# Kernel optimization log

Hardware: AMD Instinct MI355X
Metric: run time of the kernel (lower is better)

The kernel has to match this reference:

```python
import jax, jax.numpy as jnp
import numpy as np

DIM = 192          # token dim
INNER = 288        # round4(1.5*DIM)
NH_Q = 72          # headwise-proj heads (INNER // qkv_block_size)
DH_Q = 4           # per-head dim of q/k/v projections
NH_M = 4           # mLSTM heads (= qkv_block_size)
DH_M = 72          # INNER // NH_M
H, W = 32, 32
S = H * W
B = 8
KS = 3             # conv kernel size
EPS = 1e-6
LN_EPS = 1e-5


def setup_inputs() -> dict:
    key = jax.random.key(0)
    ks = jax.random.split(key, 12)
    sc = 0.02
    return {
        "x": jax.random.normal(ks[0], (B, S, DIM), jnp.float32),
        "proj_up_w": jax.random.normal(ks[1], (2 * INNER, DIM), jnp.float32) * sc,
        "q_w": jax.random.normal(ks[2], (NH_Q, DH_Q, DH_Q), jnp.float32) * sc,
        "k_w": jax.random.normal(ks[3], (NH_Q, DH_Q, DH_Q), jnp.float32) * sc,
        "v_w": jax.random.normal(ks[4], (NH_Q, DH_Q, DH_Q), jnp.float32) * sc,
        "conv_w": jax.random.normal(ks[5], (KS, KS, 1, INNER), jnp.float32) * sc,  # depthwise HWIO
        "ig_w": jax.random.normal(ks[6], (NH_M, 3 * INNER), jnp.float32) * sc,
        "ig_b": jax.random.normal(ks[7], (NH_M,), jnp.float32) * 0.1,
        "fg_w": jax.random.normal(ks[8], (NH_M, 3 * INNER), jnp.float32) * sc,
        "fg_b": jnp.linspace(3.0, 6.0, NH_M, dtype=jnp.float32),  # original fgate bias init
        "norm_w": jnp.ones((INNER,), jnp.float32),
        "skip": jnp.ones((INNER,), jnp.float32),
        "proj_down_w": jax.random.normal(ks[9], (DIM, INNER), jnp.float32) * sc,
    }


def _headwise(x, w):
    # x: (B,S,INNER), w: (NH_Q, DH_Q, DH_Q); block-diagonal linear per head
    xh = x.reshape(*x.shape[:-1], NH_Q, DH_Q)
    return jnp.einsum("bshd,hod->bsho", xh, w).reshape(x.shape)


def _mlstm_parallel(q, k, v, ig, fg):
    # q,k,v: (B,NH,S,DH); ig,fg: (B,NH,S) gate preactivations
    Ss, DH = q.shape[2], q.shape[3]
    logf = jax.nn.log_sigmoid(fg)                 # (B,NH,S)
    lfc = jnp.cumsum(logf, axis=-1)               # (B,NH,S)
    logF = lfc[..., :, None] - lfc[..., None, :]  # (B,NH,S,S): sum of logf over (j, i]
    mask = jnp.tril(jnp.ones((Ss, Ss), bool))
    logD = jnp.where(mask, logF + ig[..., None, :], -jnp.inf)
    maxD = jnp.max(logD, axis=-1, keepdims=True)  # (B,NH,S,1)
    Dm = jnp.exp(logD - maxD)
    qk = jnp.einsum("bnsd,bntd->bnst", q, k) / jnp.sqrt(jnp.float32(DH))
    Cm = qk * Dm
    normalizer = jnp.maximum(jnp.abs(Cm.sum(-1, keepdims=True)), jnp.exp(-maxD))
    return jnp.einsum("bnst,bntd->bnsd", Cm / (normalizer + EPS), v)


def reference(x, proj_up_w, q_w, k_w, v_w, conv_w, ig_w, ig_b, fg_w, fg_b,
              norm_w, skip, proj_down_w):
    Bb, Ss, _ = x.shape
    y = x @ proj_up_w.T                               # (B,S,2*INNER)
    x_m, z = y[..., :INNER], y[..., INNER:]
    # depthwise 2d conv over the (H,W) token grid
    xc = x_m.reshape(Bb, H, W, INNER)
    xc = jax.lax.conv_general_dilated(
        xc, conv_w, (1, 1), "SAME",
        dimension_numbers=("NHWC", "HWIO", "NHWC"), feature_group_count=INNER)
    xc = xc.reshape(Bb, Ss, INNER)
    xa = jax.nn.silu(xc)
    q = _headwise(xa, q_w)
    k = _headwise(xa, k_w)
    v = _headwise(x_m, v_w)
    gate_in = jnp.concatenate([q, k, v], axis=-1)      # (B,S,3*INNER)
    ig = (gate_in @ ig_w.T + ig_b).transpose(0, 2, 1)  # (B,NH_M,S)
    fg = (gate_in @ fg_w.T + fg_b).transpose(0, 2, 1)
    qh = q.reshape(Bb, Ss, NH_M, DH_M).transpose(0, 2, 1, 3)
    kh = k.reshape(Bb, Ss, NH_M, DH_M).transpose(0, 2, 1, 3)
    vh = v.reshape(Bb, Ss, NH_M, DH_M).transpose(0, 2, 1, 3)
    h = _mlstm_parallel(qh, kh, vh, ig, fg)            # (B,NH_M,S,DH_M)
    # per-head layernorm (group norm with NH_M groups), weight per channel
    mu = h.mean(-1, keepdims=True)
    var = h.var(-1, keepdims=True)
    hn = (h - mu) / jnp.sqrt(var + LN_EPS)
    hn = hn * norm_w.reshape(NH_M, 1, DH_M)[None]
    hn = hn.transpose(0, 2, 1, 3).reshape(Bb, Ss, INNER)
    h_skip = hn + skip * xa
    h_state = h_skip * jax.nn.silu(z)
    return h_state @ proj_down_w.T
```

## Files before the change

### kernel.cpp

```cpp
#include <hip/hip_runtime.h>
#include <math.h>

#define B_ 8
#define S_ 1024
#define INNER_ 288
#define NHM_ 4
#define DHM_ 72
#define H_ 32
#define W_ 32

typedef unsigned short ushort_t;
typedef unsigned int uint_t;
typedef __bf16 bf16x8 __attribute__((ext_vector_type(8)));
typedef float f32x4 __attribute__((ext_vector_type(4)));

__device__ __forceinline__ ushort_t f2bf(float f) {
  union { float f; unsigned u; } v; v.f = f;
  unsigned r = v.u + 0x7FFF + ((v.u >> 16) & 1);
  return (ushort_t)(r >> 16);
}
__device__ __forceinline__ float bf2f(ushort_t u) {
  union { unsigned u; float f; } v; v.u = ((unsigned)u) << 16;
  return v.f;
}
__device__ __forceinline__ void gl16(const void* g, void* l) {
  __builtin_amdgcn_global_load_lds(
      (const __attribute__((address_space(1))) void*)g,
      (__attribute__((address_space(3))) void*)l, 16, 0, 0);
}

__global__ __launch_bounds__(256) void cvt_swz_kernel(
    const float* __restrict__ src, ushort_t* __restrict__ dst, int K, int KPAD) {
  const int idx = blockIdx.x * 256 + threadIdx.x;
  const int k = idx % KPAD, m = idx / KPAD;
  const float v = (k < K) ? src[(size_t)m * K + k] : 0.f;
  dst[(size_t)m * KPAD + (k & ~63) + ((k & 63) ^ ((m & 7) << 3))] = f2bf(v);
}

template<int KT>
__global__ __launch_bounds__(256) void gemm_bf16(
    const ushort_t* __restrict__ A, const ushort_t* __restrict__ Bw,
    float* __restrict__ C, int N) {
  __shared__ __align__(16) ushort_t As[2][128 * 64];
  __shared__ __align__(16) ushort_t Bs[2][64 * 64];
  const int tid = threadIdx.x, lane = tid & 63, wv = tid >> 6;
  const int wm = wv >> 1, wn = wv & 1;
  const int cl = lane & 15, rowb = lane >> 4;
  const int m0 = blockIdx.y * 128, n0 = blockIdx.x * 64;
  const char* Ab = (const char*)A;
  const char* Bb = (const char*)Bw;

  auto stage = [&](int buf, int kt) {
    for (int u = wv; u < 24; u += 4) {
      if (u < 16) {
        const int o = u * 1024 + lane * 16;
        const int r = o >> 7, c = o & 127;
        gl16(Ab + ((size_t)(m0 + r) * KT + kt) * 128 + c, (char*)As[buf] + u * 1024);
      } else {
        const int o = (u - 16) * 1024 + lane * 16;
        const int r = o >> 7, c = o & 127;
        gl16(Bb + ((size_t)(n0 + r) * KT + kt) * 128 + c, (char*)Bs[buf] + (u - 16) * 1024);
      }
    }
  };

  f32x4 acc[4][2];
#pragma unroll
  for (int mi = 0; mi < 4; ++mi)
#pragma unroll
    for (int nj = 0; nj < 2; ++nj) acc[mi][nj] = (f32x4){0.f, 0.f, 0.f, 0.f};

  stage(0, 0);
  __syncthreads();
  for (int kt = 0; kt < KT; ++kt) {
    const int cur = kt & 1;
    if (kt + 1 < KT) stage(cur ^ 1, kt + 1);
#pragma unroll
    for (int ks = 0; ks < 2; ++ks) {
      bf16x8 af[4], bfr[2];
#pragma unroll
      for (int mi = 0; mi < 4; ++mi) {
        const int row = wm * 64 + mi * 16 + cl;
        af[mi] = *(const bf16x8*)((const char*)As[cur] + row * 128 +
                                  ((2 * (ks * 32 + rowb * 8)) ^ ((row & 7) << 4)));
      }
#pragma unroll
      for (int nj = 0; nj < 2; ++nj) {
        const int row = wn * 32 + nj * 16 + cl;
        bfr[nj] = *(const bf16x8*)((const char*)Bs[cur] + row * 128 +
                                   ((2 * (ks * 32 + rowb * 8)) ^ ((row & 7) << 4)));
      }
#pragma unroll
      for (int mi = 0; mi < 4; ++mi)
#pragma unroll
        for (int nj = 0; nj < 2; ++nj)
          acc[mi][nj] = __builtin_amdgcn_mfma_f32_16x16x32_bf16(af[mi], bfr[nj], acc[mi][nj], 0, 0, 0);
    }
    __syncthreads();
  }
#pragma unroll
  for (int mi = 0; mi < 4; ++mi)
#pragma unroll
    for (int i = 0; i < 4; ++i) {
      const size_t m = m0 + wm * 64 + mi * 16 + rowb * 4 + i;
#pragma unroll
      for (int nj = 0; nj < 2; ++nj)
        C[m * N + n0 + wn * 32 + nj * 16 + cl] = acc[mi][nj][i];
    }
}

__global__ __launch_bounds__(256) void conv_silu_kernel(
    const float* __restrict__ y, const float* __restrict__ cw, float* __restrict__ xa) {
  const int idx = blockIdx.x * 256 + threadIdx.x;
  const int c4 = idx % 72;
  const int p = idx / 72;
  const int c = c4 * 4;
  const int xx = p & 31, yy = (p >> 5) & 31, b = p >> 10;
  float4 acc = {0.f, 0.f, 0.f, 0.f};
#pragma unroll
  for (int ky = 0; ky < 3; ++ky) {
    const int iy = yy + ky - 1;
    if (iy < 0 || iy >= H_) continue;
#pragma unroll
    for (int kx = 0; kx < 3; ++kx) {
      const int ix = xx + kx - 1;
      if (ix < 0 || ix >= W_) continue;
      const float4 v = *(const float4*)&y[((size_t)((b << 10) + (iy << 5) + ix)) * 576 + c];
      const float4 w = *(const float4*)&cw[(ky * 3 + kx) * INNER_ + c];
      acc.x += v.x * w.x; acc.y += v.y * w.y; acc.z += v.z * w.z; acc.w += v.w * w.w;
    }
  }
  float4 o;
  o.x = acc.x / (1.f + __expf(-acc.x));
  o.y = acc.y / (1.f + __expf(-acc.y));
  o.z = acc.z / (1.f + __expf(-acc.z));
  o.w = acc.w / (1.f + __expf(-acc.w));
  *(float4*)&xa[(size_t)p * INNER_ + c] = o;
}

__global__ __launch_bounds__(256) void headwise_kernel(
    const float* __restrict__ y, const float* __restrict__ xa,
    const float* __restrict__ qw, const float* __restrict__ kw, const float* __restrict__ vw,
    ushort_t* __restrict__ qg, ushort_t* __restrict__ kg, ushort_t* __restrict__ vg) {
  const int idx = blockIdx.x * 256 + threadIdx.x;
  const int g = idx & 31, r = idx >> 5;
  const int s = r & 1023, bn = r >> 10, b = bn >> 2, n = bn & 3;
  const int swz = (r & 7) << 3;
  ushort_t* qrow = qg + (size_t)r * 128;
  ushort_t* krow = kg + (size_t)r * 128;
  if (g >= 18) {
    const int d0 = 72 + (g - 18) * 4;
    const ushort4 z = {0, 0, 0, 0};
    *(ushort4*)&qrow[d0 ^ swz] = z;
    *(ushort4*)&krow[d0 ^ swz] = z;
    return;
  }
  const int hq = n * 18 + g;
  const int p = (b << 10) + s;
  const float4 xav = *(const float4*)&xa[(size_t)p * INNER_ + hq * 4];
  const float4 xmv = *(const float4*)&y[(size_t)p * 576 + hq * 4];
  float q[4], k2[4], v[4];
#pragma unroll
  for (int o = 0; o < 4; ++o) {
    const float4 wq = *(const float4*)&qw[hq * 16 + o * 4];
    const float4 wk = *(const float4*)&kw[hq * 16 + o * 4];
    const float4 wv4 = *(const float4*)&vw[hq * 16 + o * 4];
    q[o]  = wq.x * xav.x + wq.y * xav.y + wq.z * xav.z + wq.w * xav.w;
    k2[o] = wk.x * xav.x + wk.y * xav.y + wk.z * xav.z + wk.w * xav.w;
    v[o]  = wv4.x * xmv.x + wv4.y * xmv.y + wv4.z * xmv.z + wv4.w * xmv.w;
  }
  ushort4 uq = {f2bf(q[0]), f2bf(q[1]), f2bf(q[2]), f2bf(q[3])};
  ushort4 uk = {f2bf(k2[0]), f2bf(k2[1]), f2bf(k2[2]), f2bf(k2[3])};
  ushort4 uv = {f2bf(v[0]), f2bf(v[1]), f2bf(v[2]), f2bf(v[3])};
  *(ushort4*)&qrow[(g * 4) ^ swz] = uq;
  *(ushort4*)&krow[(g * 4) ^ swz] = uk;
  *(ushort4*)&vg[(size_t)r * 72 + g * 4] = uv;
}

__global__ __launch_bounds__(256) void vtrans_kernel(
    const ushort_t* __restrict__ vg, ushort_t* __restrict__ vtg) {
  __shared__ ushort_t T[64][82];
  const int bn = blockIdx.x >> 4, tt = blockIdx.x & 15;
  const int s0 = tt << 6, tid = threadIdx.x;
  const uint_t* v32 = (const uint_t*)vg;
  for (int i = tid; i < 64 * 36; i += 256) {
    const int rr = i / 36, c2 = i % 36;
    *(uint_t*)&T[rr][c2 * 2] = v32[((size_t)(bn * 1024 + s0 + rr)) * 36 + c2];
  }
  __syncthreads();
  char* outb = (char*)(vtg + ((size_t)(bn * 16 + tt)) * 5120);
  for (int i = tid; i < 80 * 32; i += 256) {
    const int d = i >> 5, m = i & 31;
    uint_t val;
    if (d < 72) val = (uint_t)T[2 * m][d] | ((uint_t)T[2 * m + 1][d] << 16);
    else val = (d == 72) ? 0x3F803F80u : 0u;
    *(uint_t*)(outb + d * 128 + ((m * 4) ^ ((d & 7) << 4))) = val;
  }
}

__global__ __launch_bounds__(256) void gates_kernel(
    const ushort_t* __restrict__ qg, const ushort_t* __restrict__ kg, const ushort_t* __restrict__ vg,
    const float* __restrict__ igw, const float* __restrict__ igb,
    const float* __restrict__ fgw, const float* __restrict__ fgb,
    float* __restrict__ ig, float* __restrict__ fg) {
  const int gw = (blockIdx.x * 256 + threadIdx.x) >> 6;
  const int lane = threadIdx.x & 63;
  const int b = gw >> 10, s = gw & 1023;
  float iacc[4] = {}, facc[4] = {};
  for (int j = lane; j < 864; j += 64) {
    const int part = j / INNER_;
    const int c = j - part * INNER_;
    const int n = c / DHM_, d = c % DHM_;
    const size_t row = (size_t)(b * 4 + n) * 1024 + s;
    ushort_t u;
    if (part == 2)      u = vg[row * 72 + d];
    else {
      const size_t si = row * 128 + (d ^ ((row & 7) << 3));
      u = (part == 0) ? qg[si] : kg[si];
    }
    const float gv = bf2f(u);
#pragma unroll
    for (int nn = 0; nn < 4; ++nn) {
      iacc[nn] += gv * igw[nn * 864 + j];
      facc[nn] += gv * fgw[nn * 864 + j];
    }
  }
#pragma unroll
  for (int off = 32; off >= 1; off >>= 1) {
#pragma unroll
    for (int nn = 0; nn < 4; ++nn) {
      iacc[nn] += __shfl_xor(iacc[nn], off);
      facc[nn] += __shfl_xor(facc[nn], off);
    }
  }
  if (lane == 0) {
#pragma unroll
    for (int nn = 0; nn < 4; ++nn) {
      ig[((size_t)b * NHM_ + nn) * S_ + s] = iacc[nn] + igb[nn];
      fg[((size_t)b * NHM_ + nn) * S_ + s] = facc[nn] + fgb[nn];
    }
  }
}

__global__ __launch_bounds__(256) void scan_kernel(
    const float* __restrict__ fg, const float* __restrict__ ig,
    float* __restrict__ lfc, float* __restrict__ g, float* __restrict__ Mb) {
  __shared__ float sd[256];
  const int bn = blockIdx.x;
  const int tid = threadIdx.x;
  const float* fgp = &fg[(size_t)bn * S_];
  const float* igp = &ig[(size_t)bn * S_];
  float lf[4];
#pragma unroll
  for (int i = 0; i < 4; ++i) {
    const float f = fgp[tid * 4 + i];
    lf[i] = (f >= 0.f) ? -log1pf(expf(-f)) : (f - log1pf(expf(f)));
  }
  float p[4];
  p[0] = lf[0]; p[1] = p[0] + lf[1]; p[2] = p[1] + lf[2]; p[3] = p[2] + lf[3];
  sd[tid] = p[3];
  __syncthreads();
  for (int off = 1; off < 256; off <<= 1) {
    const float v = (tid >= off) ? sd[tid - off] : 0.f;
    __syncthreads();
    sd[tid] += v;
    __syncthreads();
  }
  const float excl = sd[tid] - p[3];
  float l[4];
#pragma unroll
  for (int i = 0; i < 4; ++i) {
    l[i] = excl + p[i];
    lfc[(size_t)bn * S_ + tid * 4 + i] = l[i];
  }
  float gv[4], pm[4];
#pragma unroll
  for (int i = 0; i < 4; ++i) gv[i] = igp[tid * 4 + i] - l[i];
  pm[0] = gv[0];
#pragma unroll
  for (int i = 1; i < 4; ++i) pm[i] = fmaxf(pm[i - 1], gv[i]);
  __syncthreads();
  sd[tid] = pm[3];
  __syncthreads();
  for (int off = 1; off < 256; off <<= 1) {
    const float v = (tid >= off) ? sd[tid - off] : -INFINITY;
    __syncthreads();
    sd[tid] = fmaxf(sd[tid], v);
    __syncthreads();
  }
  const float exclm = (tid > 0) ? sd[tid - 1] : -INFINITY;
#pragma unroll
  for (int i = 0; i < 4; ++i) {
    g[(size_t)bn * S_ + tid * 4 + i] = gv[i];
    Mb[(size_t)bn * S_ + tid * 4 + i] = fmaxf(exclm, pm[i]);
  }
}

__global__ __launch_bounds__(256) void mlstm_mfma(
    const ushort_t* __restrict__ qg, const ushort_t* __restrict__ kg,
    const ushort_t* __restrict__ vtg,
    const float* __restrict__ gb, const float* __restrict__ Mb, const float* __restrict__ lfc,
    float* __restrict__ hb) {
  __shared__ __align__(16) ushort_t Ks[2][64 * 128];
  __shared__ __align__(16) ushort_t Vt[2][80 * 64];
  __shared__ __align__(16) ushort_t Ps[64 * 72];
  __shared__ float gs[1024];
  __shared__ float Ms_s[64], en_s[64];
  const int bi = blockIdx.x;
  const int bn = bi & 31;
  const int j = (bi >> 5) & 7;
  const int st = (bi >> 8) ? (15 - j) : j;
  const int s0 = st << 6;
  const int tid = threadIdx.x, lane = tid & 63, wv = tid >> 6;
  const int cl = lane & 15, rowb = lane >> 4;
  const char* kb = (const char*)(kg + (size_t)bn * 1024 * 128);
  const char* vtb = (const char*)(vtg + (size_t)bn * 16 * 5120);

  auto stage = [&](int buf, int tt) {
    const char* ks = kb + (size_t)tt * (64 * 256);
    const char* vs = vtb + (size_t)tt * 10240;
    for (int u = wv; u < 26; u += 4) {
      if (u < 16) gl16(ks + u * 1024 + lane * 16, (char*)Ks[buf] + u * 1024);
      else        gl16(vs + (u - 16) * 1024 + lane * 16, (char*)Vt[buf] + (u - 16) * 1024);
    }
  };

  stage(0, 0);
  *(float4*)&gs[tid * 4] = *(const float4*)&gb[(size_t)bn * S_ + tid * 4];
  if (tid < 64) {
    const float m = Mb[(size_t)bn * S_ + s0 + tid];
    Ms_s[tid] = m;
    en_s[tid] = __expf(-(lfc[(size_t)bn * S_ + s0 + tid] + m));
  }
  const int qrow = bn * 1024 + s0 + 16 * wv + cl;
  const ushort_t* qp = qg + (size_t)qrow * 128;
  const int qx = (qrow & 7) << 3;
  bf16x8 qf[3];
#pragma unroll
  for (int kk = 0; kk < 3; ++kk) qf[kk] = *(const bf16x8*)&qp[(kk * 32 + rowb * 8) ^ qx];

  f32x4 accv[5];
#pragma unroll
  for (int n0 = 0; n0 < 5; ++n0) accv[n0] = (f32x4){0.f, 0.f, 0.f, 0.f};
  const float rsc = 0.11785113019775793f;
  const int srl0 = 16 * wv + 4 * rowb;
  __syncthreads();

  for (int tt = 0; tt < st; ++tt) {
    const int cur = tt & 1;
    stage(cur ^ 1, tt + 1);
    const int t0 = tt << 6;
    f32x4 qk[4];
#pragma unroll
    for (int n0 = 0; n0 < 4; ++n0) qk[n0] = (f32x4){0.f, 0.f, 0.f, 0.f};
#pragma unroll
    for (int kk = 0; kk < 3; ++kk) {
#pragma unroll
      for (int n0 = 0; n0 < 4; ++n0) {
        const int rl = n0 * 16 + cl;
        const bf16x8 b = *(const bf16x8*)((const char*)Ks[cur] + rl * 256 +
                                          ((2 * (kk * 32 + rowb * 8)) ^ ((rl & 7) << 4)));
        qk[n0] = __builtin_amdgcn_mfma_f32_16x16x32_bf16(qf[kk], b, qk[n0], 0, 0, 0);
      }
    }
#pragma unroll
    for (int n0 = 0; n0 < 4; ++n0) {
      const float gtv = gs[t0 + n0 * 16 + cl];
#pragma unroll
      for (int i = 0; i < 4; ++i) {
        const float w = qk[n0][i] * rsc * __expf(gtv - Ms_s[srl0 + i]);
        Ps[(srl0 + i) * 72 + n0 * 16 + cl] = f2bf(w);
      }
    }
#pragma unroll
    for (int k0 = 0; k0 < 64; k0 += 32) {
      const bf16x8 a = *(const bf16x8*)&Ps[(16 * wv + cl) * 72 + k0 + rowb * 8];
#pragma unroll
      for (int n0 = 0; n0 < 5; ++n0) {
        const int d = n0 * 16 + cl;
        const bf16x8 b = *(const bf16x8*)((const char*)Vt[cur] + d * 128 +
                                          ((2 * (k0 + rowb * 8)) ^ ((d & 7) << 4)));
        accv[n0] = __builtin_amdgcn_mfma_f32_16x16x32_bf16(a, b, accv[n0], 0, 0, 0);
      }
    }
    __syncthreads();
  }
  {
    const int cur = st & 1;
    f32x4 qk[4];
#pragma unroll
    for (int n0 = 0; n0 < 4; ++n0) qk[n0] = (f32x4){0.f, 0.f, 0.f, 0.f};
#pragma unroll
    for (int kk = 0; kk < 3; ++kk) {
#pragma unroll
      for (int n0 = 0; n0 < 4; ++n0) {
        const int rl = n0 * 16 + cl;
        const bf16x8 b = *(const bf16x8*)((const char*)Ks[cur] + rl * 256 +
                                          ((2 * (kk * 32 + rowb * 8)) ^ ((rl & 7) << 4)));
        qk[n0] = __builtin_amdgcn_mfma_f32_16x16x32_bf16(qf[kk], b, qk[n0], 0, 0, 0);
      }
    }
#pragma unroll
    for (int n0 = 0; n0 < 4; ++n0) {
      const int tc = n0 * 16 + cl;
      const float gtv = gs[s0 + tc];
#pragma unroll
      for (int i = 0; i < 4; ++i) {
        const int srl = srl0 + i;
        const float w = (tc <= srl) ? qk[n0][i] * rsc * __expf(gtv - Ms_s[srl]) : 0.f;
        Ps[srl * 72 + n0 * 16 + cl] = f2bf(w);
      }
    }
#pragma unroll
    for (int k0 = 0; k0 < 64; k0 += 32) {
      const bf16x8 a = *(const bf16x8*)&Ps[(16 * wv + cl) * 72 + k0 + rowb * 8];
#pragma unroll
      for (int n0 = 0; n0 < 5; ++n0) {
        const int d = n0 * 16 + cl;
        const bf16x8 b = *(const bf16x8*)((const char*)Vt[cur] + d * 128 +
                                          ((2 * (k0 + rowb * 8)) ^ ((d & 7) << 4)));
        accv[n0] = __builtin_amdgcn_mfma_f32_16x16x32_bf16(a, b, accv[n0], 0, 0, 0);
      }
    }
  }
  float inv[4];
#pragma unroll
  for (int i = 0; i < 4; ++i) {
    const float rs = __shfl(accv[4][i], (lane & 48) + 8, 64);
    inv[i] = 1.f / (fmaxf(fabsf(rs), en_s[srl0 + i]) + 1e-6f);
  }
  float* hp = hb + ((size_t)bn * S_ + s0) * DHM_;
#pragma unroll
  for (int n0 = 0; n0 < 5; ++n0) {
    const int d = n0 * 16 + cl;
    if (d < 72) {
#pragma unroll
      for (int i = 0; i < 4; ++i)
        hp[(size_t)(srl0 + i) * DHM_ + d] = accv[n0][i] * inv[i];
    }
  }
}

__global__ __launch_bounds__(256) void ln_fuse_kernel(
    const float* __restrict__ hb, const float* __restrict__ xa, const float* __restrict__ y,
    const float* __restrict__ normw, const float* __restrict__ skipw,
    ushort_t* __restrict__ hsb) {
  const int gw = (blockIdx.x * 256 + threadIdx.x) >> 6;
  const int lane = threadIdx.x & 63;
  const int n = gw & 3;
  const int p = gw >> 2;
  const int b = p >> 10, s = p & 1023;
  const int pswz = (p & 7) << 3;
  ushort_t* hrow = hsb + (size_t)p * 320;
  const float* hp = hb + (((size_t)b * NHM_ + n) * S_ + s) * DHM_;
  const float x1 = hp[lane];
  const float x2 = (lane < 8) ? hp[64 + lane] : 0.f;
  float sum = x1 + x2;
#pragma unroll
  for (int off = 32; off >= 1; off >>= 1) sum += __shfl_xor(sum, off);
  const float mean = sum * (1.f / 72.f);
  const float d1 = x1 - mean;
  const float d2 = (lane < 8) ? (x2 - mean) : 0.f;
  float ss = d1 * d1 + d2 * d2;
#pragma unroll
  for (int off = 32; off >= 1; off >>= 1) ss += __shfl_xor(ss, off);
  const float inv = rsqrtf(ss * (1.f / 72.f) + 1e-5f);
  {
    const int c = n * DHM_ + lane;
    const float hn = d1 * inv * normw[c];
    const float xav = xa[(size_t)p * INNER_ + c];
    const float z = y[(size_t)p * 576 + 288 + c];
    const float sz = z / (1.f + __expf(-z));
    hrow[(c & ~63) + ((c & 63) ^ pswz)] = f2bf((hn + skipw[c] * xav) * sz);
  }
  if (lane < 8) {
    const int c = n * DHM_ + 64 + lane;
    const float hn = d2 * inv * normw[c];
    const float xav = xa[(size_t)p * INNER_ + c];
    const float z = y[(size_t)p * 576 + 288 + c];
    const float sz = z / (1.f + __expf(-z));
    hrow[(c & ~63) + ((c & 63) ^ pswz)] = f2bf((hn + skipw[c] * xav) * sz);
  }
  if (n == 3 && lane >= 32) {
    const int c = 288 + (lane - 32);
    hrow[256 + ((c & 63) ^ pswz)] = 0;
  }
}

extern "C" void kernel_launch(void* const* d_in, const int* in_sizes, int n_in,
                              void* d_out, int out_size, void* d_ws, size_t ws_size,
                              hipStream_t stream) {
  const float* x           = (const float*)d_in[0];
  const float* proj_up_w   = (const float*)d_in[1];
  const float* q_w         = (const float*)d_in[2];
  const float* k_w         = (const float*)d_in[3];
  const float* v_w         = (const float*)d_in[4];
  const float* conv_w      = (const float*)d_in[5];
  const float* ig_w        = (const float*)d_in[6];
  const float* ig_b        = (const float*)d_in[7];
  const float* fg_w        = (const float*)d_in[8];
  const float* fg_b        = (const float*)d_in[9];
  const float* norm_w      = (const float*)d_in[10];
  const float* skipw       = (const float*)d_in[11];
  const float* proj_down_w = (const float*)d_in[12];
  float* out = (float*)d_out;

  float* ws = (float*)d_ws;
  float* y      = ws;
  float* xa     = y      + (size_t)8192 * 576;
  float* igb_   = xa     + (size_t)8192 * 288;
  float* fgb_   = igb_   + 32768;
  float* lfcb   = fgb_   + 32768;
  float* gbuf   = lfcb   + 32768;
  float* Mbuf   = gbuf   + 32768;
  float* hbuf   = Mbuf   + 32768;
  ushort_t* qg  = (ushort_t*)(hbuf + (size_t)8192 * 288);
  ushort_t* kg  = qg  + (size_t)32 * 1024 * 128;
  ushort_t* vg  = kg  + (size_t)32 * 1024 * 128;
  ushort_t* vtg = vg  + (size_t)32 * 1024 * 72;
  ushort_t* xbf = vtg + (size_t)32 * 16 * 5120;
  ushort_t* wup = xbf + (size_t)8192 * 192;
  ushort_t* wdn = wup + (size_t)576 * 192;
  ushort_t* hsb = wdn + (size_t)192 * 320;

  cvt_swz_kernel<<<(8192 * 192) / 256, 256, 0, stream>>>(x, xbf, 192, 192);
  cvt_swz_kernel<<<(576 * 192) / 256, 256, 0, stream>>>(proj_up_w, wup, 192, 192);
  cvt_swz_kernel<<<(192 * 320) / 256, 256, 0, stream>>>(proj_down_w, wdn, 288, 320);
  gemm_bf16<3><<<dim3(9, 64), 256, 0, stream>>>(xbf, wup, y, 576);
  conv_silu_kernel<<<(8192 * 72) / 256, 256, 0, stream>>>(y, conv_w, xa);
  headwise_kernel<<<(32768 * 32) / 256, 256, 0, stream>>>(y, xa, q_w, k_w, v_w, qg, kg, vg);
  vtrans_kernel<<<512, 256, 0, stream>>>(vg, vtg);
  gates_kernel<<<8192 / 4, 256, 0, stream>>>(qg, kg, vg, ig_w, ig_b, fg_w, fg_b, igb_, fgb_);
  scan_kernel<<<B_ * NHM_, 256, 0, stream>>>(fgb_, igb_, lfcb, gbuf, Mbuf);
  mlstm_mfma<<<512, 256, 0, stream>>>(qg, kg, vtg, gbuf, Mbuf, lfcb, hbuf);
  ln_fuse_kernel<<<(8192 * 4) / 4, 256, 0, stream>>>(hbuf, xa, y, norm_w, skipw, hsb);
  gemm_bf16<5><<<dim3(3, 64), 256, 0, stream>>>(hsb, wdn, out, 192);
}
```

Measured before the change: 183.0 us.

## Fuse conv+headwise, fold layernorm into mLSTM epilogue, merge prep conversions

Merges the three fp32-to-bf16 conversion launches and the zero-padding of q/k/hsb into one vectorized prep kernel. Merges the depthwise conv+SiLU with the headwise q/k/v projection so xa and the centre tap are reused from registers. Moves the per-head layernorm, skip, SiLU gate and bf16 store into the mLSTM kernel epilogue, removing the fp32 h buffer round trip and a launch. The epilogue now does 16-lane shuffle reductions and scattered 2-byte stores inside the heavy attention kernel, which may add register pressure there.

New measurement: 168.9 us. 7.7% less time.

```diff
diff --git a/kernel.cpp b/kernel.cpp
--- a/kernel.cpp
+++ b/kernel.cpp
@@ -29,12 +29,56 @@
       (__attribute__((address_space(3))) void*)l, 16, 0, 0);
 }
 
-__global__ __launch_bounds__(256) void cvt_swz_kernel(
-    const float* __restrict__ src, ushort_t* __restrict__ dst, int K, int KPAD) {
-  const int idx = blockIdx.x * 256 + threadIdx.x;
-  const int k = idx % KPAD, m = idx / KPAD;
-  const float v = (k < K) ? src[(size_t)m * K + k] : 0.f;
-  dst[(size_t)m * KPAD + (k & ~63) + ((k & 63) ^ ((m & 7) << 3))] = f2bf(v);
+__global__ __launch_bounds__(256) void prep_kernel(
+    const float* __restrict__ x, const float* __restrict__ wupf,
+    const float* __restrict__ wdnf,
+    ushort_t* __restrict__ xbf, ushort_t* __restrict__ wup, ushort_t* __restrict__ wdn,
+    ushort_t* __restrict__ hsb, ushort_t* __restrict__ qg, ushort_t* __restrict__ kg) {
+  int s4 = blockIdx.x * 256 + threadIdx.x;
+  const ushort4 z4 = {0, 0, 0, 0};
+  if (s4 < 393216) {
+    const int m = s4 / 48, k4 = (s4 % 48) * 4;
+    const float4 v = *(const float4*)&x[(size_t)m * 192 + k4];
+    ushort4 w = {f2bf(v.x), f2bf(v.y), f2bf(v.z), f2bf(v.w)};
+    *(ushort4*)&xbf[(size_t)m * 192 + (k4 & ~63) + ((k4 & 63) ^ ((m & 7) << 3))] = w;
+    return;
+  }
+  s4 -= 393216;
+  if (s4 < 27648) {
+    const int m = s4 / 48, k4 = (s4 % 48) * 4;
+    const float4 v = *(const float4*)&wupf[(size_t)m * 192 + k4];
+    ushort4 w = {f2bf(v.x), f2bf(v.y), f2bf(v.z), f2bf(v.w)};
+    *(ushort4*)&wup[(size_t)m * 192 + (k4 & ~63) + ((k4 & 63) ^ ((m & 7) << 3))] = w;
+    return;
+  }
+  s4 -= 27648;
+  if (s4 < 15360) {
+    const int m = s4 / 80, k4 = (s4 % 80) * 4;
+    ushort4 w = z4;
+    if (k4 < 288) {
+      const float4 v = *(const float4*)&wdnf[(size_t)m * 288 + k4];
+      w = (ushort4){f2bf(v.x), f2bf(v.y), f2bf(v.z), f2bf(v.w)};
+    }
+    *(ushort4*)&wdn[(size_t)m * 320 + (k4 & ~63) + ((k4 & 63) ^ ((m & 7) << 3))] = w;
+    return;
+  }
+  s4 -= 15360;
+  if (s4 < 131072) {
+    const int p = s4 >> 4, j = s4 & 15;
+    *(ushort4*)&hsb[(size_t)p * 320 + 256 + j * 4] = z4;
+    return;
+  }
+  s4 -= 131072;
+  if (s4 < 524288) {
+    const int r = s4 >> 4, j = s4 & 15;
+    *(ushort4*)&qg[(size_t)r * 128 + 64 + j * 4] = z4;
+    return;
+  }
+  s4 -= 524288;
+  {
+    const int r = s4 >> 4, j = s4 & 15;
+    *(ushort4*)&kg[(size_t)r * 128 + 64 + j * 4] = z4;
+  }
 }
 
 template<int KT>
@@ -109,14 +153,18 @@
     }
 }
 
-__global__ __launch_bounds__(256) void conv_silu_kernel(
-    const float* __restrict__ y, const float* __restrict__ cw, float* __restrict__ xa) {
+__global__ __launch_bounds__(256) void conv_head_kernel(
+    const float* __restrict__ y, const float* __restrict__ cw,
+    const float* __restrict__ qw, const float* __restrict__ kw, const float* __restrict__ vw,
+    float* __restrict__ xa,
+    ushort_t* __restrict__ qg, ushort_t* __restrict__ kg, ushort_t* __restrict__ vg) {
   const int idx = blockIdx.x * 256 + threadIdx.x;
-  const int c4 = idx % 72;
+  const int hq = idx % 72;
   const int p = idx / 72;
-  const int c = c4 * 4;
-  const int xx = p & 31, yy = (p >> 5) & 31, b = p >> 10;
+  const int c = hq * 4;
+  const int xx = p & 31, yy = (p >> 5) & 31, b = p >> 10, s = p & 1023;
   float4 acc = {0.f, 0.f, 0.f, 0.f};
+  float4 xmv;
 #pragma unroll
   for (int ky = 0; ky < 3; ++ky) {
     const int iy = yy + ky - 1;
@@ -126,54 +174,35 @@
       const int ix = xx + kx - 1;
       if (ix < 0 || ix >= W_) continue;
       const float4 v = *(const float4*)&y[((size_t)((b << 10) + (iy << 5) + ix)) * 576 + c];
+      if (ky == 1 && kx == 1) xmv = v;
       const float4 w = *(const float4*)&cw[(ky * 3 + kx) * INNER_ + c];
       acc.x += v.x * w.x; acc.y += v.y * w.y; acc.z += v.z * w.z; acc.w += v.w * w.w;
     }
   }
-  float4 o;
-  o.x = acc.x / (1.f + __expf(-acc.x));
-  o.y = acc.y / (1.f + __expf(-acc.y));
-  o.z = acc.z / (1.f + __expf(-acc.z));
-  o.w = acc.w / (1.f + __expf(-acc.w));
-  *(float4*)&xa[(size_t)p * INNER_ + c] = o;
-}
-
-__global__ __launch_bounds__(256) void headwise_kernel(
-    const float* __restrict__ y, const float* __restrict__ xa,
-    const float* __restrict__ qw, const float* __restrict__ kw, const float* __restrict__ vw,
-    ushort_t* __restrict__ qg, ushort_t* __restrict__ kg, ushort_t* __restrict__ vg) {
-  const int idx = blockIdx.x * 256 + threadIdx.x;
-  const int g = idx & 31, r = idx >> 5;
-  const int s = r & 1023, bn = r >> 10, b = bn >> 2, n = bn & 3;
-  const int swz = (r & 7) << 3;
-  ushort_t* qrow = qg + (size_t)r * 128;
-  ushort_t* krow = kg + (size_t)r * 128;
-  if (g >= 18) {
-    const int d0 = 72 + (g - 18) * 4;
-    const ushort4 z = {0, 0, 0, 0};
-    *(ushort4*)&qrow[d0 ^ swz] = z;
-    *(ushort4*)&krow[d0 ^ swz] = z;
-    return;
-  }
-  const int hq = n * 18 + g;
-  const int p = (b << 10) + s;
-  const float4 xav = *(const float4*)&xa[(size_t)p * INNER_ + hq * 4];
-  const float4 xmv = *(const float4*)&y[(size_t)p * 576 + hq * 4];
+  float4 xa4;
+  xa4.x = acc.x / (1.f + __expf(-acc.x));
+  xa4.y = acc.y / (1.f + __expf(-acc.y));
+  xa4.z = acc.z / (1.f + __expf(-acc.z));
+  xa4.w = acc.w / (1.f + __expf(-acc.w));
+  *(float4*)&xa[(size_t)p * INNER_ + c] = xa4;
   float q[4], k2[4], v[4];
 #pragma unroll
   for (int o = 0; o < 4; ++o) {
     const float4 wq = *(const float4*)&qw[hq * 16 + o * 4];
     const float4 wk = *(const float4*)&kw[hq * 16 + o * 4];
     const float4 wv4 = *(const float4*)&vw[hq * 16 + o * 4];
-    q[o]  = wq.x * xav.x + wq.y * xav.y + wq.z * xav.z + wq.w * xav.w;
-    k2[o] = wk.x * xav.x + wk.y * xav.y + wk.z * xav.z + wk.w * xav.w;
+    q[o]  = wq.x * xa4.x + wq.y * xa4.y + wq.z * xa4.z + wq.w * xa4.w;
+    k2[o] = wk.x * xa4.x + wk.y * xa4.y + wk.z * xa4.z + wk.w * xa4.w;
     v[o]  = wv4.x * xmv.x + wv4.y * xmv.y + wv4.z * xmv.z + wv4.w * xmv.w;
   }
+  const int n = hq / 18, g = hq % 18;
+  const int r = (b * 4 + n) * 1024 + s;
+  const int swz = (s & 7) << 3;
   ushort4 uq = {f2bf(q[0]), f2bf(q[1]), f2bf(q[2]), f2bf(q[3])};
   ushort4 uk = {f2bf(k2[0]), f2bf(k2[1]), f2bf(k2[2]), f2bf(k2[3])};
   ushort4 uv = {f2bf(v[0]), f2bf(v[1]), f2bf(v[2]), f2bf(v[3])};
-  *(ushort4*)&qrow[(g * 4) ^ swz] = uq;
-  *(ushort4*)&krow[(g * 4) ^ swz] = uk;
+  *(ushort4*)&qg[(size_t)r * 128 + ((g * 4) ^ swz)] = uq;
+  *(ushort4*)&kg[(size_t)r * 128 + ((g * 4) ^ swz)] = uk;
   *(ushort4*)&vg[(size_t)r * 72 + g * 4] = uv;
 }
 
@@ -300,7 +329,9 @@
     const ushort_t* __restrict__ qg, const ushort_t* __restrict__ kg,
     const ushort_t* __restrict__ vtg,
     const float* __restrict__ gb, const float* __restrict__ Mb, const float* __restrict__ lfc,
-    float* __restrict__ hb) {
+    const float* __restrict__ xa, const float* __restrict__ y,
+    const float* __restrict__ normw, const float* __restrict__ skipw,
+    ushort_t* __restrict__ hsb) {
   __shared__ __align__(16) ushort_t Ks[2][64 * 128];
   __shared__ __align__(16) ushort_t Vt[2][80 * 64];
   __shared__ __align__(16) ushort_t Ps[64 * 72];
@@ -429,61 +460,48 @@
     const float rs = __shfl(accv[4][i], (lane & 48) + 8, 64);
     inv[i] = 1.f / (fmaxf(fabsf(rs), en_s[srl0 + i]) + 1e-6f);
   }
-  float* hp = hb + ((size_t)bn * S_ + s0) * DHM_;
+  const int b = bn >> 2, n = bn & 3;
+  float nw[5], sw[5];
 #pragma unroll
   for (int n0 = 0; n0 < 5; ++n0) {
     const int d = n0 * 16 + cl;
-    if (d < 72) {
-#pragma unroll
-      for (int i = 0; i < 4; ++i)
-        hp[(size_t)(srl0 + i) * DHM_ + d] = accv[n0][i] * inv[i];
-    }
-  }
-}
-
-__global__ __launch_bounds__(256) void ln_fuse_kernel(
-    const float* __restrict__ hb, const float* __restrict__ xa, const float* __restrict__ y,
-    const float* __restrict__ normw, const float* __restrict__ skipw,
-    ushort_t* __restrict__ hsb) {
-  const int gw = (blockIdx.x * 256 + threadIdx.x) >> 6;
-  const int lane = threadIdx.x & 63;
-  const int n = gw & 3;
-  const int p = gw >> 2;
-  const int b = p >> 10, s = p & 1023;
-  const int pswz = (p & 7) << 3;
-  ushort_t* hrow = hsb + (size_t)p * 320;
-  const float* hp = hb + (((size_t)b * NHM_ + n) * S_ + s) * DHM_;
-  const float x1 = hp[lane];
-  const float x2 = (lane < 8) ? hp[64 + lane] : 0.f;
-  float sum = x1 + x2;
-#pragma unroll
-  for (int off = 32; off >= 1; off >>= 1) sum += __shfl_xor(sum, off);
-  const float mean = sum * (1.f / 72.f);
-  const float d1 = x1 - mean;
-  const float d2 = (lane < 8) ? (x2 - mean) : 0.f;
-  float ss = d1 * d1 + d2 * d2;
-#pragma unroll
-  for (int off = 32; off >= 1; off >>= 1) ss += __shfl_xor(ss, off);
-  const float inv = rsqrtf(ss * (1.f / 72.f) + 1e-5f);
-  {
-    const int c = n * DHM_ + lane;
-    const float hn = d1 * inv * normw[c];
-    const float xav = xa[(size_t)p * INNER_ + c];
-    const float z = y[(size_t)p * 576 + 288 + c];
-    const float sz = z / (1.f + __expf(-z));
-    hrow[(c & ~63) + ((c & 63) ^ pswz)] = f2bf((hn + skipw[c] * xav) * sz);
-  }
-  if (lane < 8) {
-    const int c = n * DHM_ + 64 + lane;
-    const float hn = d2 * inv * normw[c];
-    const float xav = xa[(size_t)p * INNER_ + c];
-    const float z = y[(size_t)p * 576 + 288 + c];
-    const float sz = z / (1.f + __expf(-z));
-    hrow[(c & ~63) + ((c & 63) ^ pswz)] = f2bf((hn + skipw[c] * xav) * sz);
-  }
-  if (n == 3 && lane >= 32) {
-    const int c = 288 + (lane - 32);
-    hrow[256 + ((c & 63) ^ pswz)] = 0;
+    nw[n0] = (d < 72) ? normw[n * 72 + d] : 0.f;
+    sw[n0] = (d < 72) ? skipw[n * 72 + d] : 0.f;
+  }
+#pragma unroll
+  for (int i = 0; i < 4; ++i) {
+    const int srl = srl0 + i;
+    const int p = (b << 10) + s0 + srl;
+    float hv[5];
+#pragma unroll
+    for (int n0 = 0; n0 < 5; ++n0) hv[n0] = accv[n0][i] * inv[i];
+    float hsum = hv[0] + hv[1] + hv[2] + hv[3] + ((cl < 8) ? hv[4] : 0.f);
+#pragma unroll
+    for (int m = 1; m < 16; m <<= 1) hsum += __shfl_xor(hsum, m);
+    const float mean = hsum * (1.f / 72.f);
+    float dsq = 0.f;
+#pragma unroll
+    for (int n0 = 0; n0 < 5; ++n0) {
+      const int d = n0 * 16 + cl;
+      const float dd = hv[n0] - mean;
+      if (d < 72) dsq += dd * dd;
+    }
+#pragma unroll
+    for (int m = 1; m < 16; m <<= 1) dsq += __shfl_xor(dsq, m);
+    const float rstd = rsqrtf(dsq * (1.f / 72.f) + 1e-5f);
+    const int pswz = (p & 7) << 3;
+#pragma unroll
+    for (int n0 = 0; n0 < 5; ++n0) {
+      const int d = n0 * 16 + cl;
+      if (d < 72) {
+        const int c = n * 72 + d;
+        const float hn = (hv[n0] - mean) * rstd * nw[n0];
+        const float xav = xa[(size_t)p * INNER_ + c];
+        const float z = y[(size_t)p * 576 + 288 + c];
+        const float sz = z / (1.f + __expf(-z));
+        hsb[(size_t)p * 320 + (c & ~63) + ((c & 63) ^ pswz)] = f2bf((hn + sw[n0] * xav) * sz);
+      }
+    }
   }
 }
 
@@ -513,8 +531,7 @@
   float* lfcb   = fgb_   + 32768;
   float* gbuf   = lfcb   + 32768;
   float* Mbuf   = gbuf   + 32768;
-  float* hbuf   = Mbuf   + 32768;
-  ushort_t* qg  = (ushort_t*)(hbuf + (size_t)8192 * 288);
+  ushort_t* qg  = (ushort_t*)(Mbuf + 32768);
   ushort_t* kg  = qg  + (size_t)32 * 1024 * 128;
   ushort_t* vg  = kg  + (size_t)32 * 1024 * 128;
   ushort_t* vtg = vg  + (size_t)32 * 1024 * 72;
@@ -523,16 +540,15 @@
   ushort_t* wdn = wup + (size_t)576 * 192;
   ushort_t* hsb = wdn + (size_t)192 * 320;
 
-  cvt_swz_kernel<<<(8192 * 192) / 256, 256, 0, stream>>>(x, xbf, 192, 192);
-  cvt_swz_kernel<<<(576 * 192) / 256, 256, 0, stream>>>(proj_up_w, wup, 192, 192);
-  cvt_swz_kernel<<<(192 * 320) / 256, 256, 0, stream>>>(proj_down_w, wdn, 288, 320);
+  prep_kernel<<<6312, 256, 0, stream>>>(x, proj_up_w, proj_down_w,
+                                        xbf, wup, wdn, hsb, qg, kg);
   gemm_bf16<3><<<dim3(9, 64), 256, 0, stream>>>(xbf, wup, y, 576);
-  conv_silu_kernel<<<(8192 * 72) / 256, 256, 0, stream>>>(y, conv_w, xa);
-  headwise_kernel<<<(32768 * 32) / 256, 256, 0, stream>>>(y, xa, q_w, k_w, v_w, qg, kg, vg);
+  conv_head_kernel<<<(8192 * 72) / 256, 256, 0, stream>>>(
+      y, conv_w, q_w, k_w, v_w, xa, qg, kg, vg);
   vtrans_kernel<<<512, 256, 0, stream>>>(vg, vtg);
   gates_kernel<<<8192 / 4, 256, 0, stream>>>(qg, kg, vg, ig_w, ig_b, fg_w, fg_b, igb_, fgb_);
   scan_kernel<<<B_ * NHM_, 256, 0, stream>>>(fgb_, igb_, lfcb, gbuf, Mbuf);
-  mlstm_mfma<<<512, 256, 0, stream>>>(qg, kg, vtg, gbuf, Mbuf, lfcb, hbuf);
-  ln_fuse_kernel<<<(8192 * 4) / 4, 256, 0, stream>>>(hbuf, xa, y, norm_w, skipw, hsb);
+  mlstm_mfma<<<512, 256, 0, stream>>>(qg, kg, vtg, gbuf, Mbuf, lfcb,
+                                      xa, y, norm_w, skipw, hsb);
   gemm_bf16<5><<<dim3(3, 64), 256, 0, stream>>>(hsb, wdn, out, 192);
 }
```
